# Kernel tuning notes

Hardware: AMD Instinct MI355X
Metric: run time of the kernel (lower is better)

Reference implementation:

```python
import jax, jax.numpy as jnp
import numpy as np
from jax import lax

V, E, HD, T = 100000, 256, 512, 11
H = HD // 2
B, S = 32, 512
START, STOP = 9, 10
NEG = -10000.0


def _lstm_dir(x, h0, c0, w_ih, w_hh, b_ih, b_hh):
    # x: (time, batch, in). PyTorch gate order i, f, g, o.
    def step(carry, xt):
        h, c = carry
        g = xt @ w_ih.T + b_ih + h @ w_hh.T + b_hh
        i, f, gg, o = jnp.split(g, 4, axis=-1)
        c = jax.nn.sigmoid(f) * c + jax.nn.sigmoid(i) * jnp.tanh(gg)
        h = jax.nn.sigmoid(o) * jnp.tanh(c)
        return (h, c), h
    _, hs = lax.scan(step, (h0, c0), x)
    return hs


def _features(sentence, embed, w_ih_f, w_hh_f, b_ih_f, b_hh_f,
              w_ih_b, w_hh_b, b_ih_b, b_hh_b, h0, c0, w_out, b_out):
    x = embed[sentence]  # (B, S, E)
    # Faithful to original: torch LSTM is seq-first, so it scans over axis 0 (B)
    # with 'batch' dim S (init_hidden uses sentence.shape[1]).
    hf = _lstm_dir(x, h0[0], c0[0], w_ih_f, w_hh_f, b_ih_f, b_hh_f)
    hb = _lstm_dir(x[::-1], h0[1], c0[1], w_ih_b, w_hh_b, b_ih_b, b_hh_b)[::-1]
    out = jnp.concatenate([hf, hb], axis=-1)  # (B, S, HD)
    return out @ w_out.T + b_out  # (B, S, T)


def _viterbi(feats, transitions):
    # feats: (B, S, T); CRF treats dim0 as batch, dim1 as time (as in source).
    delta0 = jnp.full((feats.shape[0], T), NEG, feats.dtype).at[:, START].set(0.0)

    def step(delta, feat_t):
        sc = transitions[None, :, :] + delta[:, None, :]  # (B, T_to, T_from)
        new = sc.max(-1) + feat_t
        return new, jnp.argmax(sc, -1)

    feats_t = jnp.moveaxis(feats[:, 1:], 1, 0)  # (S-1, B, T)
    deltaT, psis = lax.scan(step, delta0, feats_t)
    score = deltaT.max(-1)            # (B,)
    last = jnp.argmax(deltaT, -1)     # (B,)

    def back(nxt, psi_t):
        tag = jnp.take_along_axis(psi_t, nxt[:, None], axis=-1)[:, 0]
        return tag, tag

    _, earlier = lax.scan(back, last, psis, reverse=True)  # (S-1, B)
    path = jnp.concatenate([earlier, last[None, :]], axis=0).T  # (B, S)
    return score, path


def setup_inputs() -> dict:
    key = jax.random.key(0)
    ks = jax.random.split(key, 20)
    sc = 0.05
    sentence = jax.random.randint(ks[0], (B, S), 0, V)
    embed = jax.random.normal(ks[1], (V, E), jnp.float32) * sc
    w_ih_f = jax.random.normal(ks[2], (4 * H, E), jnp.float32) * sc
    w_hh_f = jax.random.normal(ks[3], (4 * H, H), jnp.float32) * sc
    b_ih_f = jax.random.normal(ks[4], (4 * H,), jnp.float32) * sc
    b_hh_f = jax.random.normal(ks[5], (4 * H,), jnp.float32) * sc
    w_ih_b = jax.random.normal(ks[6], (4 * H, E), jnp.float32) * sc
    w_hh_b = jax.random.normal(ks[7], (4 * H, H), jnp.float32) * sc
    b_ih_b = jax.random.normal(ks[8], (4 * H,), jnp.float32) * sc
    b_hh_b = jax.random.normal(ks[9], (4 * H,), jnp.float32) * sc
    h0 = jax.random.normal(ks[10], (2, S, H), jnp.float32)
    c0 = jax.random.normal(ks[11], (2, S, H), jnp.float32)
    w_out = jax.random.normal(ks[12], (T, HD), jnp.float32) * sc
    b_out = jax.random.normal(ks[13], (T,), jnp.float32) * sc
    transitions = jax.random.normal(ks[14], (T, T), jnp.float32)
    transitions = transitions.at[START, :].set(NEG).at[:, STOP].set(NEG)
    return dict(sentence=sentence, embed=embed,
                w_ih_f=w_ih_f, w_hh_f=w_hh_f, b_ih_f=b_ih_f, b_hh_f=b_hh_f,
                w_ih_b=w_ih_b, w_hh_b=w_hh_b, b_ih_b=b_ih_b, b_hh_b=b_hh_b,
                h0=h0, c0=c0, w_out=w_out, b_out=b_out, transitions=transitions)


def reference(sentence, embed, w_ih_f, w_hh_f, b_ih_f, b_hh_f,
              w_ih_b, w_hh_b, b_ih_b, b_hh_b, h0, c0, w_out, b_out, transitions):
    feats = _features(sentence, embed, w_ih_f, w_hh_f, b_ih_f, b_hh_f,
                      w_ih_b, w_hh_b, b_ih_b, b_hh_b, h0, c0, w_out, b_out)
    return _viterbi(feats, transitions)
```

## Files before the change

### kernel.cpp

```cpp
#include <hip/hip_runtime.h>
#include <math.h>


namespace {

constexpr int T_ = 11;
constexpr int HT = 256 * 512;

__device__ __forceinline__ size_t gq_off(int t, int d, int j, int q, int s) {
  return ((((size_t)(t * 2 + d) * 256 + j) * 4 + q) * 512 + s);
}

__global__ __launch_bounds__(256) void k_prep(
    const float* __restrict__ w_ih_f, const float* __restrict__ w_ih_b,
    const float* __restrict__ w_hh_f, const float* __restrict__ w_hh_b,
    const float* __restrict__ b_ih_f, const float* __restrict__ b_hh_f,
    const float* __restrict__ b_ih_b, const float* __restrict__ b_hh_b,
    const float* __restrict__ h0, const float* __restrict__ c0,
    const float* __restrict__ w_out,
    float* __restrict__ wiq, float* __restrict__ wt4, float* __restrict__ bq,
    float* __restrict__ ct, float* __restrict__ ht_f, float* __restrict__ ht_b,
    float* __restrict__ wot) {
  const int i = blockIdx.x * 256 + threadIdx.x;
  if (i < 524288) {
    int d = i >> 18, r = i & 262143, gcr = r >> 8, k = r & 255;
    int q = gcr >> 8, j = gcr & 255;
    const float* w = d ? w_ih_b : w_ih_f;
    wiq[((size_t)(d * 256 + k) * 256 + j) * 4 + q] = w[gcr * 256 + k];
  } else if (i < 1048576) {
    int i2 = i - 524288;
    int d = i2 >> 18, r = i2 & 262143, gcr = r >> 8, k = r & 255;
    int q = gcr >> 8, j = gcr & 255;
    const float* w = d ? w_hh_b : w_hh_f;
    wt4[((size_t)(d * 256 + k) * 256 + j) * 4 + q] = w[gcr * 256 + k];
  } else if (i < 1050624) {
    int r = i - 1048576;
    int d = r >> 10, x = r & 1023, j = x >> 2, q = x & 3;
    const float* bi = d ? b_ih_b : b_ih_f;
    const float* bh = d ? b_hh_b : b_hh_f;
    bq[r] = bi[q * 256 + j] + bh[q * 256 + j];
  } else if (i < 1312768) {
    int r = i - 1050624;
    int d = r >> 17, y = r & 131071, j = y >> 9, s = y & 511;
    ct[r] = c0[((size_t)d * 512 + s) * 256 + j];
  } else if (i < 1574912) {
    int r = i - 1312768;
    int d = r >> 17, y = r & 131071, j = y >> 9, s = y & 511;
    float v = h0[((size_t)d * 512 + s) * 256 + j];
    if (d == 0) ht_f[y] = v; else ht_b[y] = v;
  } else if (i < 1580544) {
    int r = i - 1574912;
    int k = r / 11, tag = r - k * 11;
    wot[r] = w_out[tag * 512 + k];
  }
}

__global__ __launch_bounds__(256, 4) void k_ggemm(
    const int* __restrict__ sent, const float* __restrict__ embed,
    const float* __restrict__ wiq, const float* __restrict__ bq,
    float* __restrict__ Gq) {
  __shared__ float As[64][67];
  const int tid = threadIdx.x;
  const int bid = blockIdx.x;
  const int jg8 = bid & 7;
  const int d = (bid >> 3) & 1;
  const int rt = bid >> 4;
  const int wid = __builtin_amdgcn_readfirstlane(tid >> 6);
  const int lane = tid & 63;
  const int row0 = rt * 64;
  const int t = row0 >> 9;
  const int sb = (row0 & 511) + lane;
  const int j0 = (jg8 * 4 + wid) * 8;

  const int rr = tid & 63, eq = tid >> 6;
  const int tok = sent[row0 + rr];
  const float* erow = embed + (size_t)tok * 256 + eq * 16;

  float acc[32];
#pragma unroll
  for (int g = 0; g < 32; ++g) acc[g] = 0.f;

  const float* wbase = wiq + (size_t)d * 256 * 1024;

  for (int ci = 0; ci < 4; ++ci) {
    const int k0 = ci * 64;
    const float* ep = erow + k0;
    float4 v0 = *(const float4*)(ep);
    float4 v1 = *(const float4*)(ep + 4);
    float4 v2 = *(const float4*)(ep + 8);
    float4 v3 = *(const float4*)(ep + 12);
    const int kb = eq * 16;
    As[kb + 0][rr] = v0.x;  As[kb + 1][rr] = v0.y;  As[kb + 2][rr] = v0.z;  As[kb + 3][rr] = v0.w;
    As[kb + 4][rr] = v1.x;  As[kb + 5][rr] = v1.y;  As[kb + 6][rr] = v1.z;  As[kb + 7][rr] = v1.w;
    As[kb + 8][rr] = v2.x;  As[kb + 9][rr] = v2.y;  As[kb + 10][rr] = v2.z; As[kb + 11][rr] = v2.w;
    As[kb + 12][rr] = v3.x; As[kb + 13][rr] = v3.y; As[kb + 14][rr] = v3.z; As[kb + 15][rr] = v3.w;
    __syncthreads();
#pragma unroll 2
    for (int kk = 0; kk < 64; ++kk) {
      float a = As[kk][lane];
      const float* wp = wbase + (size_t)(k0 + kk) * 1024 + j0 * 4;
#pragma unroll
      for (int g = 0; g < 32; ++g) acc[g] = fmaf(a, wp[g], acc[g]);
    }
    __syncthreads();
  }
  const float* bp = bq + ((size_t)d * 256 + j0) * 4;
#pragma unroll
  for (int g = 0; g < 32; ++g) {
    int jj = g >> 2, q = g & 3;
    Gq[gq_off(t, d, j0 + jj, q, sb)] = acc[g] + bp[g];
  }
}

__global__ __launch_bounds__(512, 4) void k_rstep(
    const float* __restrict__ wt4, const float* __restrict__ Gq,
    float* __restrict__ ht_f, float* __restrict__ ht_b,
    float* __restrict__ ct, int t) {
  __shared__ float red[3][128][17];
  __shared__ float gb[4][16][33];
  const int tid = threadIdx.x;
  const int bid = blockIdx.x;
  const int jsl = bid & 15, d = (bid >> 4) & 1, sg = bid >> 5;
  const int kh = __builtin_amdgcn_readfirstlane(tid >> 7);
  const int sq = __builtin_amdgcn_readfirstlane((tid >> 6) & 1);
  const int rem = tid & 127;
  const int lane = tid & 63;
  const int j0 = jsl * 16;
  const int s0 = sg * 32 + sq * 16;
  const int tt = d ? 31 - t : t;

  float* htX = d ? ht_b : ht_f;
  const float* hprev = htX + (size_t)t * HT;
  const float* wp = wt4 + ((size_t)d * 256 + (size_t)kh * 64) * 1024 + j0 * 4 + lane;
  const float* hp = hprev + (size_t)kh * 64 * 512 + s0;

  float acc[16];
#pragma unroll
  for (int i = 0; i < 16; ++i) acc[i] = 0.f;

#pragma unroll 4
  for (int k = 0; k < 64; ++k) {
    const float w = wp[(size_t)k * 1024];
    const float* h = hp + (size_t)k * 512;
    float4 h0_ = *(const float4*)(h);
    float4 h1_ = *(const float4*)(h + 4);
    float4 h2_ = *(const float4*)(h + 8);
    float4 h3_ = *(const float4*)(h + 12);
    acc[0]  = fmaf(w, h0_.x, acc[0]);
    acc[1]  = fmaf(w, h0_.y, acc[1]);
    acc[2]  = fmaf(w, h0_.z, acc[2]);
    acc[3]  = fmaf(w, h0_.w, acc[3]);
    acc[4]  = fmaf(w, h1_.x, acc[4]);
    acc[5]  = fmaf(w, h1_.y, acc[5]);
    acc[6]  = fmaf(w, h1_.z, acc[6]);
    acc[7]  = fmaf(w, h1_.w, acc[7]);
    acc[8]  = fmaf(w, h2_.x, acc[8]);
    acc[9]  = fmaf(w, h2_.y, acc[9]);
    acc[10] = fmaf(w, h2_.z, acc[10]);
    acc[11] = fmaf(w, h2_.w, acc[11]);
    acc[12] = fmaf(w, h3_.x, acc[12]);
    acc[13] = fmaf(w, h3_.y, acc[13]);
    acc[14] = fmaf(w, h3_.z, acc[14]);
    acc[15] = fmaf(w, h3_.w, acc[15]);
  }

  if (kh > 0) {
#pragma unroll
    for (int i = 0; i < 16; ++i) red[kh - 1][rem][i] = acc[i];
  }
  __syncthreads();
  if (kh == 0) {
    const int jl = lane >> 2, q = lane & 3;
#pragma unroll
    for (int i = 0; i < 16; ++i) {
      float v = acc[i] + red[0][rem][i] + red[1][rem][i] + red[2][rem][i];
      gb[q][jl][sq * 16 + i] = v;
    }
  }
  __syncthreads();

  {
    const int jl2 = tid >> 5, sp = tid & 31;
    const int j = j0 + jl2;
    const int s = sg * 32 + sp;
    const float* gp = Gq + gq_off(tt, d, j, 0, s);
    float gi = gb[0][jl2][sp] + gp[0];
    float gf = gb[1][jl2][sp] + gp[512];
    float gg = gb[2][jl2][sp] + gp[1024];
    float go = gb[3][jl2][sp] + gp[1536];
    float si = 1.f / (1.f + expf(-gi));
    float sf = 1.f / (1.f + expf(-gf));
    float tg = tanhf(gg);
    float so = 1.f / (1.f + expf(-go));
    const size_t coff = ((size_t)d * 256 + j) * 512 + s;
    float cp = ct[coff];
    float cn = sf * cp + si * tg;
    float hn = so * tanhf(cn);
    ct[coff] = cn;
    htX[(size_t)(t + 1) * HT + (size_t)j * 512 + s] = hn;
  }
}

__global__ __launch_bounds__(256) void k_out(
    const float* __restrict__ ht_f, const float* __restrict__ ht_b,
    const float* __restrict__ wot, const float* __restrict__ b_out,
    float* __restrict__ featsT) {
  __shared__ float red[4][11][64];
  const int tid = threadIdx.x;
  const int bid = blockIdx.x;
  const int t = bid >> 3, stile = bid & 7;
  const int wid = __builtin_amdgcn_readfirstlane(tid >> 6);
  const int lane = tid & 63;
  const int s0 = stile * 64;
  const int kg0 = wid * 128;
  const float* src = (wid < 2)
      ? ht_f + (size_t)(t + 1) * HT + (size_t)kg0 * 512
      : ht_b + (size_t)(32 - t) * HT + (size_t)(kg0 - 256) * 512;

  float acc[11];
#pragma unroll
  for (int g = 0; g < 11; ++g) acc[g] = 0.f;
#pragma unroll 4
  for (int kk = 0; kk < 128; ++kk) {
    float a = src[(size_t)kk * 512 + s0 + lane];
    const float* wp = wot + (size_t)(kg0 + kk) * 11;
#pragma unroll
    for (int g = 0; g < 11; ++g) acc[g] = fmaf(a, wp[g], acc[g]);
  }
#pragma unroll
  for (int g = 0; g < 11; ++g) red[wid][g][lane] = acc[g];
  __syncthreads();
  if (wid == 0) {
#pragma unroll
    for (int g = 0; g < 11; ++g) {
      float v = red[0][g][lane] + red[1][g][lane] + red[2][g][lane] +
                red[3][g][lane] + b_out[g];
      featsT[(size_t)g * 16384 + t * 512 + s0 + lane] = v;
    }
  }
}

__global__ __launch_bounds__(128) void k_viterbi(const float* __restrict__ featsT,
                                                 const float* __restrict__ trans,
                                                 float* __restrict__ out) {
  __shared__ float fl[512 * T_];
  __shared__ unsigned char psiL[511 * T_];
  __shared__ unsigned char specL[121 * 47];
  __shared__ unsigned char selL[16];
  __shared__ int lastL;
  __shared__ float scoreL;
  const int b = blockIdx.x, tid = threadIdx.x;
  for (int i = tid; i < 512 * T_; i += 128) {
    int tag = i >> 9, s = i & 511;
    fl[s * T_ + tag] = featsT[(size_t)tag * 16384 + b * 512 + s];
  }
  __syncthreads();

  if (tid < 64) {
    const int lane = tid;
    const int to = (lane < T_) ? lane : 0;
    float tr[T_];
#pragma unroll
    for (int f = 0; f < T_; ++f) tr[f] = trans[to * T_ + f];
    float delta = (lane == 9) ? 0.f : -10000.f;

    for (int s = 1; s < 512; ++s) {
      float fv = fl[s * T_ + to];
      float v0 = tr[0] + __shfl(delta, 0, 64);
      float v1 = tr[1] + __shfl(delta, 1, 64);
      float v2 = tr[2] + __shfl(delta, 2, 64);
      float v3 = tr[3] + __shfl(delta, 3, 64);
      float v4 = tr[4] + __shfl(delta, 4, 64);
      float v5 = tr[5] + __shfl(delta, 5, 64);
      float v6 = tr[6] + __shfl(delta, 6, 64);
      float v7 = tr[7] + __shfl(delta, 7, 64);
      float v8 = tr[8] + __shfl(delta, 8, 64);
      float v9 = tr[9] + __shfl(delta, 9, 64);
      float v10 = tr[10] + __shfl(delta, 10, 64);
      float mA = fmaxf(fmaxf(v0, v1), v2);
      float mB = fmaxf(fmaxf(v3, v4), v5);
      float mC = fmaxf(fmaxf(v6, v7), v8);
      float mD = fmaxf(v9, v10);
      float m = fmaxf(fmaxf(mA, mB), fmaxf(mC, mD));
      delta = m + fv;
      unsigned msk = (v0 == m) ? 1u : 0u;
      msk |= (v1 == m) ? 2u : 0u;
      msk |= (v2 == m) ? 4u : 0u;
      msk |= (v3 == m) ? 8u : 0u;
      msk |= (v4 == m) ? 16u : 0u;
      msk |= (v5 == m) ? 32u : 0u;
      msk |= (v6 == m) ? 64u : 0u;
      msk |= (v7 == m) ? 128u : 0u;
      msk |= (v8 == m) ? 256u : 0u;
      msk |= (v9 == m) ? 512u : 0u;
      msk |= (v10 == m) ? 1024u : 0u;
      int am = __ffs(msk) - 1;
      if (lane < T_) psiL[(s - 1) * T_ + lane] = (unsigned char)am;
    }
    float d0 = __shfl(delta, 0, 64), d1 = __shfl(delta, 1, 64);
    float d2 = __shfl(delta, 2, 64), d3 = __shfl(delta, 3, 64);
    float d4 = __shfl(delta, 4, 64), d5 = __shfl(delta, 5, 64);
    float d6 = __shfl(delta, 6, 64), d7 = __shfl(delta, 7, 64);
    float d8 = __shfl(delta, 8, 64), d9 = __shfl(delta, 9, 64);
    float d10 = __shfl(delta, 10, 64);
    float mA = fmaxf(fmaxf(d0, d1), d2);
    float mB = fmaxf(fmaxf(d3, d4), d5);
    float mC = fmaxf(fmaxf(d6, d7), d8);
    float mD = fmaxf(d9, d10);
    float m = fmaxf(fmaxf(mA, mB), fmaxf(mC, mD));
    unsigned msk = (d0 == m) ? 1u : 0u;
    msk |= (d1 == m) ? 2u : 0u;
    msk |= (d2 == m) ? 4u : 0u;
    msk |= (d3 == m) ? 8u : 0u;
    msk |= (d4 == m) ? 16u : 0u;
    msk |= (d5 == m) ? 32u : 0u;
    msk |= (d6 == m) ? 64u : 0u;
    msk |= (d7 == m) ? 128u : 0u;
    msk |= (d8 == m) ? 256u : 0u;
    msk |= (d9 == m) ? 512u : 0u;
    msk |= (d10 == m) ? 1024u : 0u;
    int am = __ffs(msk) - 1;
    if (lane == 0) { lastL = am; scoreL = m; }
  }
  __syncthreads();

  const int last = lastL;
  if (tid < 121) {
    const int g = tid / 11, tau = tid - g * 11;
    const int khi = 510 - 47 * g;
    const int len = (g < 10) ? 47 : 41;
    int cur = tau;
    unsigned char* sp = &specL[(g * 11 + tau) * 47];
    for (int i = 0; i < len; ++i) {
      cur = psiL[(khi - i) * T_ + cur];
      sp[i] = (unsigned char)cur;
    }
  }
  __syncthreads();
  if (tid == 0) {
    int cur = last;
    for (int g = 0; g < 11; ++g) {
      selL[g] = (unsigned char)cur;
      int len = (g < 10) ? 47 : 41;
      cur = specL[(g * 11 + cur) * 47 + (len - 1)];
    }
    out[b] = scoreL;
    out[32 + (size_t)b * 512 + 511] = (float)last;
  }
  __syncthreads();
  if (tid < 121) {
    const int g = tid / 11, tau = tid - g * 11;
    if (tau == selL[g]) {
      const int khi = 510 - 47 * g;
      const int len = (g < 10) ? 47 : 41;
      float* path = out + 32 + (size_t)b * 512;
      const unsigned char* sp = &specL[(g * 11 + tau) * 47];
      for (int i = 0; i < len; ++i) path[khi - i] = (float)sp[i];
    }
  }
}

}

extern "C" void kernel_launch(void* const* d_in, const int* in_sizes, int n_in,
                              void* d_out, int out_size, void* d_ws, size_t ws_size,
                              hipStream_t stream) {
  const int* sent     = (const int*)d_in[0];
  const float* embed  = (const float*)d_in[1];
  const float* w_ih_f = (const float*)d_in[2];
  const float* w_hh_f = (const float*)d_in[3];
  const float* b_ih_f = (const float*)d_in[4];
  const float* b_hh_f = (const float*)d_in[5];
  const float* w_ih_b = (const float*)d_in[6];
  const float* w_hh_b = (const float*)d_in[7];
  const float* b_ih_b = (const float*)d_in[8];
  const float* b_hh_b = (const float*)d_in[9];
  const float* h0     = (const float*)d_in[10];
  const float* c0     = (const float*)d_in[11];
  const float* w_out  = (const float*)d_in[12];
  const float* b_out  = (const float*)d_in[13];
  const float* trans  = (const float*)d_in[14];

  float* ws = (float*)d_ws;
  float* Gq     = ws;
  float* ht_f   = Gq + 33554432;
  float* ht_b   = ht_f + 4325376;
  float* ct     = ht_b + 4325376;
  float* wiq    = ct + 262144;
  float* wt4    = wiq + 524288;
  float* bq     = wt4 + 524288;
  float* wot    = bq + 2048;
  float* featsT = wot + 5632;

  k_prep<<<6174, 256, 0, stream>>>(w_ih_f, w_ih_b, w_hh_f, w_hh_b,
                                   b_ih_f, b_hh_f, b_ih_b, b_hh_b,
                                   h0, c0, w_out,
                                   wiq, wt4, bq, ct, ht_f, ht_b, wot);
  k_ggemm<<<4096, 256, 0, stream>>>(sent, embed, wiq, bq, Gq);
  for (int t = 0; t < 32; ++t)
    k_rstep<<<512, 512, 0, stream>>>(wt4, Gq, ht_f, ht_b, ct, t);
  k_out<<<256, 256, 0, stream>>>(ht_f, ht_b, wot, b_out, featsT);
  k_viterbi<<<32, 128, 0, stream>>>(featsT, trans, (float*)d_out);
}
```

Measured before the change: 799.8 us.

## Shrink ggemm per-warp tile, use readlane and packed psi in viterbi

The input-gate GEMM now gives each wave 4 hidden units instead of 8, halving per-thread accumulators and doubling the grid. It also raises the inner unroll and drops the occupancy hint, aiming for better latency hiding and higher occupancy. The cost is that each embedding tile is loaded and staged through shared memory twice as often. The Viterbi forward loop replaces wave shuffles with scalar readlane broadcasts and packs four backpointer bytes into one 32-bit shared-memory store, to cut per-step latency and byte-store traffic.

```diff
diff --git a/kernel.cpp b/kernel.cpp
--- a/kernel.cpp
+++ b/kernel.cpp
@@ -9,6 +9,10 @@
 
 __device__ __forceinline__ size_t gq_off(int t, int d, int j, int q, int s) {
   return ((((size_t)(t * 2 + d) * 256 + j) * 4 + q) * 512 + s);
+}
+
+__device__ __forceinline__ float rdlane(float v, int l) {
+  return __uint_as_float(__builtin_amdgcn_readlane(__float_as_uint(v), l));
 }
 
 __global__ __launch_bounds__(256) void k_prep(
@@ -55,30 +59,30 @@
   }
 }
 
-__global__ __launch_bounds__(256, 4) void k_ggemm(
+__global__ __launch_bounds__(256) void k_ggemm(
     const int* __restrict__ sent, const float* __restrict__ embed,
     const float* __restrict__ wiq, const float* __restrict__ bq,
     float* __restrict__ Gq) {
   __shared__ float As[64][67];
   const int tid = threadIdx.x;
   const int bid = blockIdx.x;
-  const int jg8 = bid & 7;
-  const int d = (bid >> 3) & 1;
-  const int rt = bid >> 4;
+  const int jg4 = bid & 15;
+  const int d = (bid >> 4) & 1;
+  const int rt = bid >> 5;
   const int wid = __builtin_amdgcn_readfirstlane(tid >> 6);
   const int lane = tid & 63;
   const int row0 = rt * 64;
   const int t = row0 >> 9;
   const int sb = (row0 & 511) + lane;
-  const int j0 = (jg8 * 4 + wid) * 8;
+  const int j0 = (jg4 * 4 + wid) * 4;
 
   const int rr = tid & 63, eq = tid >> 6;
   const int tok = sent[row0 + rr];
   const float* erow = embed + (size_t)tok * 256 + eq * 16;
 
-  float acc[32];
-#pragma unroll
-  for (int g = 0; g < 32; ++g) acc[g] = 0.f;
+  float acc[16];
+#pragma unroll
+  for (int g = 0; g < 16; ++g) acc[g] = 0.f;
 
   const float* wbase = wiq + (size_t)d * 256 * 1024;
 
@@ -95,18 +99,18 @@
     As[kb + 8][rr] = v2.x;  As[kb + 9][rr] = v2.y;  As[kb + 10][rr] = v2.z; As[kb + 11][rr] = v2.w;
     As[kb + 12][rr] = v3.x; As[kb + 13][rr] = v3.y; As[kb + 14][rr] = v3.z; As[kb + 15][rr] = v3.w;
     __syncthreads();
-#pragma unroll 2
+#pragma unroll 4
     for (int kk = 0; kk < 64; ++kk) {
       float a = As[kk][lane];
       const float* wp = wbase + (size_t)(k0 + kk) * 1024 + j0 * 4;
 #pragma unroll
-      for (int g = 0; g < 32; ++g) acc[g] = fmaf(a, wp[g], acc[g]);
+      for (int g = 0; g < 16; ++g) acc[g] = fmaf(a, wp[g], acc[g]);
     }
     __syncthreads();
   }
   const float* bp = bq + ((size_t)d * 256 + j0) * 4;
 #pragma unroll
-  for (int g = 0; g < 32; ++g) {
+  for (int g = 0; g < 16; ++g) {
     int jj = g >> 2, q = g & 3;
     Gq[gq_off(t, d, j0 + jj, q, sb)] = acc[g] + bp[g];
   }
@@ -244,7 +248,7 @@
                                                  const float* __restrict__ trans,
                                                  float* __restrict__ out) {
   __shared__ float fl[512 * T_];
-  __shared__ unsigned char psiL[511 * T_];
+  __shared__ unsigned psiP[128][12];
   __shared__ unsigned char specL[121 * 47];
   __shared__ unsigned char selL[16];
   __shared__ int lastL;
@@ -263,20 +267,21 @@
 #pragma unroll
     for (int f = 0; f < T_; ++f) tr[f] = trans[to * T_ + f];
     float delta = (lane == 9) ? 0.f : -10000.f;
+    unsigned pk = 0;
 
     for (int s = 1; s < 512; ++s) {
       float fv = fl[s * T_ + to];
-      float v0 = tr[0] + __shfl(delta, 0, 64);
-      float v1 = tr[1] + __shfl(delta, 1, 64);
-      float v2 = tr[2] + __shfl(delta, 2, 64);
-      float v3 = tr[3] + __shfl(delta, 3, 64);
-      float v4 = tr[4] + __shfl(delta, 4, 64);
-      float v5 = tr[5] + __shfl(delta, 5, 64);
-      float v6 = tr[6] + __shfl(delta, 6, 64);
-      float v7 = tr[7] + __shfl(delta, 7, 64);
-      float v8 = tr[8] + __shfl(delta, 8, 64);
-      float v9 = tr[9] + __shfl(delta, 9, 64);
-      float v10 = tr[10] + __shfl(delta, 10, 64);
+      float v0 = tr[0] + rdlane(delta, 0);
+      float v1 = tr[1] + rdlane(delta, 1);
+      float v2 = tr[2] + rdlane(delta, 2);
+      float v3 = tr[3] + rdlane(delta, 3);
+      float v4 = tr[4] + rdlane(delta, 4);
+      float v5 = tr[5] + rdlane(delta, 5);
+      float v6 = tr[6] + rdlane(delta, 6);
+      float v7 = tr[7] + rdlane(delta, 7);
+      float v8 = tr[8] + rdlane(delta, 8);
+      float v9 = tr[9] + rdlane(delta, 9);
+      float v10 = tr[10] + rdlane(delta, 10);
       float mA = fmaxf(fmaxf(v0, v1), v2);
       float mB = fmaxf(fmaxf(v3, v4), v5);
       float mC = fmaxf(fmaxf(v6, v7), v8);
@@ -294,15 +299,22 @@
       msk |= (v8 == m) ? 256u : 0u;
       msk |= (v9 == m) ? 512u : 0u;
       msk |= (v10 == m) ? 1024u : 0u;
-      int am = __ffs(msk) - 1;
-      if (lane < T_) psiL[(s - 1) * T_ + lane] = (unsigned char)am;
-    }
-    float d0 = __shfl(delta, 0, 64), d1 = __shfl(delta, 1, 64);
-    float d2 = __shfl(delta, 2, 64), d3 = __shfl(delta, 3, 64);
-    float d4 = __shfl(delta, 4, 64), d5 = __shfl(delta, 5, 64);
-    float d6 = __shfl(delta, 6, 64), d7 = __shfl(delta, 7, 64);
-    float d8 = __shfl(delta, 8, 64), d9 = __shfl(delta, 9, 64);
-    float d10 = __shfl(delta, 10, 64);
+      unsigned am = (unsigned)(__ffs(msk) - 1);
+      const int r = (s - 1) & 3;
+      pk |= am << (r * 8);
+      if (r == 3) {
+        if (lane < T_) psiP[(s - 1) >> 2][lane] = pk;
+        pk = 0;
+      }
+    }
+    if (lane < T_) psiP[127][lane] = pk;
+
+    float d0 = rdlane(delta, 0), d1 = rdlane(delta, 1);
+    float d2 = rdlane(delta, 2), d3 = rdlane(delta, 3);
+    float d4 = rdlane(delta, 4), d5 = rdlane(delta, 5);
+    float d6 = rdlane(delta, 6), d7 = rdlane(delta, 7);
+    float d8 = rdlane(delta, 8), d9 = rdlane(delta, 9);
+    float d10 = rdlane(delta, 10);
     float mA = fmaxf(fmaxf(d0, d1), d2);
     float mB = fmaxf(fmaxf(d3, d4), d5);
     float mC = fmaxf(fmaxf(d6, d7), d8);
@@ -332,7 +344,8 @@
     int cur = tau;
     unsigned char* sp = &specL[(g * 11 + tau) * 47];
     for (int i = 0; i < len; ++i) {
-      cur = psiL[(khi - i) * T_ + cur];
+      const int k = khi - i;
+      cur = (int)((psiP[k >> 2][cur] >> ((k & 3) * 8)) & 0xffu);
       sp[i] = (unsigned char)cur;
     }
   }
@@ -396,7 +409,7 @@
                                    b_ih_f, b_hh_f, b_ih_b, b_hh_b,
                                    h0, c0, w_out,
                                    wiq, wt4, bq, ct, ht_f, ht_b, wot);
-  k_ggemm<<<4096, 256, 0, stream>>>(sent, embed, wiq, bq, Gq);
+  k_ggemm<<<8192, 256, 0, stream>>>(sent, embed, wiq, bq, Gq);
   for (int t = 0; t < 32; ++t)
     k_rstep<<<512, 512, 0, stream>>>(wt4, Gq, ht_f, ht_b, ct, t);
   k_out<<<256, 256, 0, stream>>>(ht_f, ht_b, wot, b_out, featsT);
```

Result: faster. 765.8 us (-4.3%).
